# Performance work log

Hardware: AMD Instinct MI355X
Metric: run time of the kernel (lower is better)

The kernel has to match this reference:

```python
import jax, jax.numpy as jnp
import numpy as np

EMBED_DIM = 1024
NUM_HEADS = 16
HEAD_DIM = EMBED_DIM // NUM_HEADS
B, S = 2, 2048


def setup_inputs() -> dict:
    key = jax.random.key(0)
    k = jax.random.split(key, 8)
    scale = 1.0 / np.sqrt(EMBED_DIM)
    return {
        "x": jax.random.normal(k[0], (B, S, EMBED_DIM), dtype=jnp.float32),
        "x1": jax.random.normal(k[1], (B, S, EMBED_DIM), dtype=jnp.float32),
        "x2": jax.random.normal(k[2], (B, S, EMBED_DIM), dtype=jnp.float32),
        "qkv_w": jax.random.normal(k[3], (3 * EMBED_DIM, EMBED_DIM), dtype=jnp.float32) * scale,
        "qkv_b": jnp.zeros((3 * EMBED_DIM,), dtype=jnp.float32),
        "out_w": jax.random.normal(k[4], (EMBED_DIM, EMBED_DIM), dtype=jnp.float32) * scale,
        "out_b": jnp.zeros((EMBED_DIM,), dtype=jnp.float32),
    }


def reference(x, x1, x2, qkv_w, qkv_b, out_w, out_b):
    # x1, x2 are accepted but unused, matching the torch module.
    b, s, e = x.shape
    qkv = x @ qkv_w.T + qkv_b                      # [B,S,3E]
    qkv = qkv.reshape(b, s, 3, NUM_HEADS, HEAD_DIM)
    qkv = jnp.transpose(qkv, (2, 0, 3, 1, 4))      # [3,B,H,S,D]
    q, k, v = qkv[0], qkv[1], qkv[2]
    scores = jnp.einsum("bhqd,bhkd->bhqk", q, k) / np.sqrt(HEAD_DIM)
    probs = jax.nn.sigmoid(scores)                 # [B,H,S,S]
    sample = jax.random.bernoulli(jax.random.key(42), probs).astype(probs.dtype)
    # straight-through: forward uses sample, gradient flows as identity to probs
    attn = probs + jax.lax.stop_gradient(sample - probs)
    out = jnp.einsum("bhqk,bhkd->bhqd", attn, v)   # [B,H,S,D]
    out = jnp.transpose(out, (0, 2, 1, 3)).reshape(b, s, e)
    return out @ out_w.T + out_b
```

## Files before the change

kernel.cpp:

```cpp
#include <hip/hip_runtime.h>
#include <stdint.h>

#define NB 2
#define NS 2048
#define NE 1024
#define NH 16
#define ND 64

typedef __attribute__((ext_vector_type(8))) short short8;
typedef __attribute__((ext_vector_type(4))) float f4;
typedef __attribute__((ext_vector_type(4))) unsigned short us4;

static __device__ __forceinline__ unsigned short bf16_rne(float x) {
  uint32_t u = __builtin_bit_cast(uint32_t, x);
  u += 0x7fffu + ((u >> 16) & 1u);
  return (unsigned short)(u >> 16);
}
static __device__ __forceinline__ float bf16_f32(unsigned short h) {
  uint32_t u = ((uint32_t)h) << 16;
  return __builtin_bit_cast(float, u);
}

static __device__ __forceinline__ void threefry42(uint32_t x0, uint32_t x1,
                                                  uint32_t& o0, uint32_t& o1) {
  const uint32_t ks0 = 0u, ks1 = 42u;
  const uint32_t ks2 = 0u ^ 42u ^ 0x1BD11BDAu;
  x0 += ks0; x1 += ks1;
#define TF4(a,b,c,d) \
  x0 += x1; x1 = __builtin_rotateleft32(x1, a); x1 ^= x0; \
  x0 += x1; x1 = __builtin_rotateleft32(x1, b); x1 ^= x0; \
  x0 += x1; x1 = __builtin_rotateleft32(x1, c); x1 ^= x0; \
  x0 += x1; x1 = __builtin_rotateleft32(x1, d); x1 ^= x0;
  TF4(13,15,26,6)  x0 += ks1; x1 += ks2 + 1u;
  TF4(17,29,16,24) x0 += ks2; x1 += ks0 + 2u;
  TF4(13,15,26,6)  x0 += ks0; x1 += ks1 + 3u;
  TF4(17,29,16,24) x0 += ks1; x1 += ks2 + 4u;
  TF4(13,15,26,6)  x0 += ks2; x1 += ks0 + 5u;
#undef TF4
  o0 = x0; o1 = x1;
}

static __device__ __forceinline__ void gl2lds16(const void* g, void* l) {
  __builtin_amdgcn_global_load_lds(
      (const __attribute__((address_space(1))) uint32_t*)g,
      (__attribute__((address_space(3))) uint32_t*)l, 16, 0, 0);
}

__global__ void k_split(const float* __restrict__ x, const float* __restrict__ qw,
                        const float* __restrict__ ow,
                        unsigned short* __restrict__ xh, unsigned short* __restrict__ xl,
                        unsigned short* __restrict__ wh, unsigned short* __restrict__ wl,
                        unsigned short* __restrict__ woh) {
  for (uint32_t i = blockIdx.x * 256u + threadIdx.x; i < 8388608u; i += gridDim.x * 256u) {
    if (i < 4194304u) {
      float v = x[i];
      unsigned short hi = bf16_rne(v);
      xh[i] = hi;
      xl[i] = bf16_rne(v - bf16_f32(hi));
    } else if (i < 7340032u) {
      uint32_t j = i - 4194304u;
      float v = qw[j];
      unsigned short hi = bf16_rne(v);
      wh[j] = hi;
      wl[j] = bf16_rne(v - bf16_f32(hi));
    } else {
      uint32_t j = i - 7340032u;
      woh[j] = bf16_rne(ow[j]);
    }
  }
}

__global__ __launch_bounds__(256) void k_qkv(
    const unsigned short* __restrict__ xh, const unsigned short* __restrict__ xl,
    const unsigned short* __restrict__ wh, const unsigned short* __restrict__ wl,
    const float* __restrict__ qkv_b,
    unsigned short* __restrict__ Qh, unsigned short* __restrict__ Ql,
    unsigned short* __restrict__ Kh, unsigned short* __restrict__ Kl,
    unsigned short* __restrict__ Vt) {
  __shared__ unsigned short Ah[128 * 32], Al[128 * 32], Bh[128 * 32], Bl[128 * 32];
  const int tid = threadIdx.x;
  const int lane = tid & 63, wid = tid >> 6;
  const int wm = wid >> 1, wn = wid & 1;
  const int bn = blockIdx.x, bm = blockIdx.y;
  const int quad = lane >> 4, c16 = lane & 15;
  const int ldrow = lane >> 2;
  const int ldk = (lane & 3) * 8;

  f4 acc[4][4];
#pragma unroll
  for (int a = 0; a < 4; ++a)
#pragma unroll
    for (int b = 0; b < 4; ++b) { f4 z = {0.f, 0.f, 0.f, 0.f}; acc[a][b] = z; }

  for (int kt = 0; kt < 32; ++kt) {
    const int k0 = kt * 32;
    __syncthreads();
#pragma unroll
    for (int r = 0; r < 2; ++r) {
      const int c = wid + r * 4;
      const int grow = c * 16 + ldrow;
      const size_t ao = (size_t)(bm * 128 + grow) * 1024 + k0 + ldk;
      const size_t bo = (size_t)(bn * 128 + grow) * 1024 + k0 + ldk;
      const int lo = c * 512 + lane * 8;
      gl2lds16(xh + ao, &Ah[lo]);
      gl2lds16(xl + ao, &Al[lo]);
      gl2lds16(wh + bo, &Bh[lo]);
      gl2lds16(wl + bo, &Bl[lo]);
    }
    __syncthreads();

    short8 ah[4], al[4], bhf[4], blf[4];
#pragma unroll
    for (int t = 0; t < 4; ++t) {
      ah[t] = *(const short8*)&Ah[(wm * 64 + t * 16 + c16) * 32 + quad * 8];
      al[t] = *(const short8*)&Al[(wm * 64 + t * 16 + c16) * 32 + quad * 8];
      bhf[t] = *(const short8*)&Bh[(wn * 64 + t * 16 + c16) * 32 + quad * 8];
      blf[t] = *(const short8*)&Bl[(wn * 64 + t * 16 + c16) * 32 + quad * 8];
    }
#pragma unroll
    for (int tm = 0; tm < 4; ++tm)
#pragma unroll
      for (int tn = 0; tn < 4; ++tn) {
        acc[tm][tn] = __builtin_amdgcn_mfma_f32_16x16x32_bf16(ah[tm], bhf[tn], acc[tm][tn], 0, 0, 0);
        acc[tm][tn] = __builtin_amdgcn_mfma_f32_16x16x32_bf16(ah[tm], blf[tn], acc[tm][tn], 0, 0, 0);
        acc[tm][tn] = __builtin_amdgcn_mfma_f32_16x16x32_bf16(al[tm], bhf[tn], acc[tm][tn], 0, 0, 0);
      }
  }

#pragma unroll
  for (int tm = 0; tm < 4; ++tm) {
#pragma unroll
    for (int tn = 0; tn < 4; ++tn) {
      const int j = bn * 128 + wn * 64 + tn * 16 + c16;
      const float bias = qkv_b[j];
      const int which = j >> 10;
      const int rem = j & 1023;
      const int h = rem >> 6, d = rem & 63;
#pragma unroll
      for (int r = 0; r < 4; ++r) {
        const int i = bm * 128 + wm * 64 + tm * 16 + quad * 4 + r;
        const int b = i >> 11, s = i & 2047;
        const int bh = b * 16 + h;
        const float v = acc[tm][tn][r] + bias;
        if (which == 2) {
          Vt[((size_t)bh * 64 + d) * 2048 + s] = bf16_rne(v);
        } else {
          const size_t off = ((size_t)bh * 2048 + s) * 64 + d;
          const unsigned short hi = bf16_rne(v);
          const unsigned short lo = bf16_rne(v - bf16_f32(hi));
          if (which == 0) { Qh[off] = hi; Ql[off] = lo; }
          else            { Kh[off] = hi; Kl[off] = lo; }
        }
      }
    }
  }
}

__global__ __launch_bounds__(256) void k_attn(
    const unsigned short* __restrict__ Qh, const unsigned short* __restrict__ Ql,
    const unsigned short* __restrict__ Khg, const unsigned short* __restrict__ Klg,
    const unsigned short* __restrict__ Vtg, unsigned short* __restrict__ AO) {
  __shared__ unsigned short Ksh[4096], Ksl[4096], Vs[4096], Pm[4096];
  const int tid = threadIdx.x;
  const int lane = tid & 63, w = tid >> 6;
  const int quad = lane >> 4, c16 = lane & 15;
  const int q0 = blockIdx.x * 64;
  const int bh = blockIdx.y;
  const size_t base = (size_t)bh * (size_t)(2048 * 64);

  const size_t qoff = base + (size_t)(q0 + w * 16 + c16) * 64 + quad * 8;
  const short8 qh0 = *(const short8*)&Qh[qoff];
  const short8 qh1 = *(const short8*)&Qh[qoff + 32];
  const short8 ql0 = *(const short8*)&Ql[qoff];
  const short8 ql1 = *(const short8*)&Ql[qoff + 32];

  const uint32_t fb = (uint32_t)bh * 4194304u +
                      (uint32_t)(q0 + w * 16 + quad * 4) * 2048u + (uint32_t)c16;

  f4 oacc[4];
#pragma unroll
  for (int s = 0; s < 4; ++s) { f4 z = {0.f, 0.f, 0.f, 0.f}; oacc[s] = z; }

  for (int kt = 0; kt < 32; ++kt) {
    const int kb = kt * 64;
    const size_t koff = base + (size_t)kb * 64;
    __syncthreads();
#pragma unroll
    for (int rd = 0; rd < 2; ++rd) {
      const int lo = rd * 2048 + tid * 8;
      gl2lds16(Khg + koff + lo, &Ksh[lo]);
      gl2lds16(Klg + koff + lo, &Ksl[lo]);
      const int cid = rd * 256 + tid;
      const int vr = cid >> 3, vc = (cid & 7) * 8;
      gl2lds16(Vtg + base + (size_t)vr * 2048 + kb + vc, &Vs[cid * 8]);
    }
    __syncthreads();

    f4 sacc[4];
#pragma unroll
    for (int sub = 0; sub < 4; ++sub) {
      const int br = (sub * 16 + c16) * 64 + quad * 8;
      const short8 kh0 = *(const short8*)&Ksh[br];
      const short8 kh1 = *(const short8*)&Ksh[br + 32];
      const short8 kl0 = *(const short8*)&Ksl[br];
      const short8 kl1 = *(const short8*)&Ksl[br + 32];
      f4 s = {0.f, 0.f, 0.f, 0.f};
      s = __builtin_amdgcn_mfma_f32_16x16x32_bf16(qh0, kh0, s, 0, 0, 0);
      s = __builtin_amdgcn_mfma_f32_16x16x32_bf16(qh1, kh1, s, 0, 0, 0);
      s = __builtin_amdgcn_mfma_f32_16x16x32_bf16(qh0, kl0, s, 0, 0, 0);
      s = __builtin_amdgcn_mfma_f32_16x16x32_bf16(qh1, kl1, s, 0, 0, 0);
      s = __builtin_amdgcn_mfma_f32_16x16x32_bf16(ql0, kh0, s, 0, 0, 0);
      s = __builtin_amdgcn_mfma_f32_16x16x32_bf16(ql1, kh1, s, 0, 0, 0);
      sacc[sub] = s;
    }

#pragma unroll
    for (int sub = 0; sub < 4; ++sub) {
#pragma unroll
      for (int r = 0; r < 4; ++r) {
        const uint32_t f = fb + (uint32_t)(r * 2048) + (uint32_t)(kb + sub * 16);
        uint32_t o0, o1;
        threefry42(0u, f, o0, o1);
        const float m = (float)((o0 ^ o1) >> 9);
        const float e = __expf(sacc[sub][r] * -0.125f);
        const float p23 = 8388608.0f * __builtin_amdgcn_rcpf(1.0f + e);
        Pm[(w * 16 + quad * 4 + r) * 64 + sub * 16 + c16] = (m < p23) ? 0x3F80u : 0u;
      }
    }

    const int pr = (w * 16 + c16) * 64 + quad * 8;
    const short8 pa0 = *(const short8*)&Pm[pr];
    const short8 pa1 = *(const short8*)&Pm[pr + 32];
#pragma unroll
    for (int sub = 0; sub < 4; ++sub) {
      const int vr = (sub * 16 + c16) * 64 + quad * 8;
      const short8 vb0 = *(const short8*)&Vs[vr];
      const short8 vb1 = *(const short8*)&Vs[vr + 32];
      oacc[sub] = __builtin_amdgcn_mfma_f32_16x16x32_bf16(pa0, vb0, oacc[sub], 0, 0, 0);
      oacc[sub] = __builtin_amdgcn_mfma_f32_16x16x32_bf16(pa1, vb1, oacc[sub], 0, 0, 0);
    }
  }

  const int b = bh >> 4, hh = bh & 15;
#pragma unroll
  for (int sub = 0; sub < 4; ++sub)
#pragma unroll
    for (int r = 0; r < 4; ++r) {
      const int srow = b * 2048 + q0 + w * 16 + quad * 4 + r;
      AO[(size_t)srow * 1024 + hh * 64 + sub * 16 + c16] = bf16_rne(oacc[sub][r]);
    }
}

__global__ __launch_bounds__(256) void k_out(
    const unsigned short* __restrict__ A, const unsigned short* __restrict__ Bw,
    const float* __restrict__ out_b, float* __restrict__ out) {
  __shared__ unsigned short As[128 * 32], Bs[128 * 32];
  const int tid = threadIdx.x;
  const int lane = tid & 63, wid = tid >> 6;
  const int wm = wid >> 1, wn = wid & 1;
  const int bn = blockIdx.x, bm = blockIdx.y;
  const int quad = lane >> 4, c16 = lane & 15;
  const int ldrow = lane >> 2;
  const int ldk = (lane & 3) * 8;

  f4 acc[4][4];
#pragma unroll
  for (int a = 0; a < 4; ++a)
#pragma unroll
    for (int b = 0; b < 4; ++b) { f4 z = {0.f, 0.f, 0.f, 0.f}; acc[a][b] = z; }

  for (int kt = 0; kt < 32; ++kt) {
    const int k0 = kt * 32;
    __syncthreads();
#pragma unroll
    for (int r = 0; r < 2; ++r) {
      const int c = wid + r * 4;
      const int grow = c * 16 + ldrow;
      const size_t ao = (size_t)(bm * 128 + grow) * 1024 + k0 + ldk;
      const size_t bo = (size_t)(bn * 128 + grow) * 1024 + k0 + ldk;
      const int lo = c * 512 + lane * 8;
      gl2lds16(A + ao, &As[lo]);
      gl2lds16(Bw + bo, &Bs[lo]);
    }
    __syncthreads();

    short8 af[4], bf[4];
#pragma unroll
    for (int t = 0; t < 4; ++t) {
      af[t] = *(const short8*)&As[(wm * 64 + t * 16 + c16) * 32 + quad * 8];
      bf[t] = *(const short8*)&Bs[(wn * 64 + t * 16 + c16) * 32 + quad * 8];
    }
#pragma unroll
    for (int tm = 0; tm < 4; ++tm)
#pragma unroll
      for (int tn = 0; tn < 4; ++tn)
        acc[tm][tn] = __builtin_amdgcn_mfma_f32_16x16x32_bf16(af[tm], bf[tn], acc[tm][tn], 0, 0, 0);
  }

#pragma unroll
  for (int tm = 0; tm < 4; ++tm) {
#pragma unroll
    for (int tn = 0; tn < 4; ++tn) {
      const int j = bn * 128 + wn * 64 + tn * 16 + c16;
      const float bias = out_b[j];
#pragma unroll
      for (int r = 0; r < 4; ++r) {
        const int i = bm * 128 + wm * 64 + tm * 16 + quad * 4 + r;
        out[(size_t)i * 1024 + j] = acc[tm][tn][r] + bias;
      }
    }
  }
}

extern "C" void kernel_launch(void* const* d_in, const int* in_sizes, int n_in,
                              void* d_out, int out_size, void* d_ws, size_t ws_size,
                              hipStream_t stream) {
  const float* x     = (const float*)d_in[0];
  const float* qkv_w = (const float*)d_in[3];
  const float* qkv_b = (const float*)d_in[4];
  const float* out_w = (const float*)d_in[5];
  const float* out_b = (const float*)d_in[6];
  float* out = (float*)d_out;

  unsigned short* xh  = (unsigned short*)d_ws;
  unsigned short* xl  = xh + 4194304;
  unsigned short* wh  = xl + 4194304;
  unsigned short* wl  = wh + 3145728;
  unsigned short* woh = wl + 3145728;
  unsigned short* Vt  = woh + 1048576;
  unsigned short* Qh  = Vt + 4194304;
  unsigned short* Ql  = Qh + 4194304;
  unsigned short* Kh  = Ql + 4194304;
  unsigned short* Kl  = Kh + 4194304;
  unsigned short* AO  = xh;

  k_split<<<8192, 256, 0, stream>>>(x, qkv_w, out_w, xh, xl, wh, wl, woh);
  k_qkv<<<dim3(24, 32), 256, 0, stream>>>(xh, xl, wh, wl, qkv_b, Qh, Ql, Kh, Kl, Vt);
  k_attn<<<dim3(32, 32), 256, 0, stream>>>(Qh, Ql, Kh, Kl, Vt, AO);
  k_out<<<dim3(8, 32), 256, 0, stream>>>(AO, woh, out_b, out);
}
```

Measured before the change: 532.7 us.

## Prefetch K/V tiles during attention, swizzle LDS, skip split-bf16 for V projection

The attention kernel now copies each K/V tile from LDS into registers, then issues the global-to-LDS load for the next tile, so the copy overlaps with the QK MFMAs and the sigmoid/Bernoulli step. The K, V and P shared tiles use an XOR-style rotated layout to cut LDS bank conflicts. The sigmoid threshold test is rewritten to drop the reciprocal. In the QKV GEMM, V-column blocks skip the low-part bf16 loads and MFMAs, and V is transposed through LDS so Vt is written with coalesced 16-byte stores. The costs are higher register pressure from holding 24 short8 fragments, and V computed at lower precision. The rewritten comparison can also flip a sample at the boundary.

Result: faster. 520.2 us (-2.4%).

```diff
diff --git a/kernel.cpp b/kernel.cpp
--- a/kernel.cpp
+++ b/kernel.cpp
@@ -77,11 +77,16 @@
     unsigned short* __restrict__ Qh, unsigned short* __restrict__ Ql,
     unsigned short* __restrict__ Kh, unsigned short* __restrict__ Kl,
     unsigned short* __restrict__ Vt) {
-  __shared__ unsigned short Ah[128 * 32], Al[128 * 32], Bh[128 * 32], Bl[128 * 32];
+  __shared__ unsigned short SM[16384];
+  unsigned short* Ah = SM;
+  unsigned short* Al = SM + 4096;
+  unsigned short* Bh = SM + 8192;
+  unsigned short* Bl = SM + 12288;
   const int tid = threadIdx.x;
   const int lane = tid & 63, wid = tid >> 6;
   const int wm = wid >> 1, wn = wid & 1;
   const int bn = blockIdx.x, bm = blockIdx.y;
+  const bool isV = (bn >= 16);
   const int quad = lane >> 4, c16 = lane & 15;
   const int ldrow = lane >> 2;
   const int ldk = (lane & 3) * 8;
@@ -103,9 +108,11 @@
       const size_t bo = (size_t)(bn * 128 + grow) * 1024 + k0 + ldk;
       const int lo = c * 512 + lane * 8;
       gl2lds16(xh + ao, &Ah[lo]);
-      gl2lds16(xl + ao, &Al[lo]);
       gl2lds16(wh + bo, &Bh[lo]);
-      gl2lds16(wl + bo, &Bl[lo]);
+      if (!isV) {
+        gl2lds16(xl + ao, &Al[lo]);
+        gl2lds16(wl + bo, &Bl[lo]);
+      }
     }
     __syncthreads();
 
@@ -113,45 +120,82 @@
 #pragma unroll
     for (int t = 0; t < 4; ++t) {
       ah[t] = *(const short8*)&Ah[(wm * 64 + t * 16 + c16) * 32 + quad * 8];
-      al[t] = *(const short8*)&Al[(wm * 64 + t * 16 + c16) * 32 + quad * 8];
       bhf[t] = *(const short8*)&Bh[(wn * 64 + t * 16 + c16) * 32 + quad * 8];
-      blf[t] = *(const short8*)&Bl[(wn * 64 + t * 16 + c16) * 32 + quad * 8];
-    }
-#pragma unroll
-    for (int tm = 0; tm < 4; ++tm)
+      if (!isV) {
+        al[t] = *(const short8*)&Al[(wm * 64 + t * 16 + c16) * 32 + quad * 8];
+        blf[t] = *(const short8*)&Bl[(wn * 64 + t * 16 + c16) * 32 + quad * 8];
+      }
+    }
+    if (isV) {
+#pragma unroll
+      for (int tm = 0; tm < 4; ++tm)
+#pragma unroll
+        for (int tn = 0; tn < 4; ++tn)
+          acc[tm][tn] = __builtin_amdgcn_mfma_f32_16x16x32_bf16(ah[tm], bhf[tn], acc[tm][tn], 0, 0, 0);
+    } else {
+#pragma unroll
+      for (int tm = 0; tm < 4; ++tm)
+#pragma unroll
+        for (int tn = 0; tn < 4; ++tn) {
+          acc[tm][tn] = __builtin_amdgcn_mfma_f32_16x16x32_bf16(ah[tm], bhf[tn], acc[tm][tn], 0, 0, 0);
+          acc[tm][tn] = __builtin_amdgcn_mfma_f32_16x16x32_bf16(ah[tm], blf[tn], acc[tm][tn], 0, 0, 0);
+          acc[tm][tn] = __builtin_amdgcn_mfma_f32_16x16x32_bf16(al[tm], bhf[tn], acc[tm][tn], 0, 0, 0);
+        }
+    }
+  }
+
+  if (!isV) {
+#pragma unroll
+    for (int tm = 0; tm < 4; ++tm) {
 #pragma unroll
       for (int tn = 0; tn < 4; ++tn) {
-        acc[tm][tn] = __builtin_amdgcn_mfma_f32_16x16x32_bf16(ah[tm], bhf[tn], acc[tm][tn], 0, 0, 0);
-        acc[tm][tn] = __builtin_amdgcn_mfma_f32_16x16x32_bf16(ah[tm], blf[tn], acc[tm][tn], 0, 0, 0);
-        acc[tm][tn] = __builtin_amdgcn_mfma_f32_16x16x32_bf16(al[tm], bhf[tn], acc[tm][tn], 0, 0, 0);
-      }
-  }
-
-#pragma unroll
-  for (int tm = 0; tm < 4; ++tm) {
-#pragma unroll
-    for (int tn = 0; tn < 4; ++tn) {
-      const int j = bn * 128 + wn * 64 + tn * 16 + c16;
-      const float bias = qkv_b[j];
-      const int which = j >> 10;
-      const int rem = j & 1023;
-      const int h = rem >> 6, d = rem & 63;
-#pragma unroll
-      for (int r = 0; r < 4; ++r) {
-        const int i = bm * 128 + wm * 64 + tm * 16 + quad * 4 + r;
-        const int b = i >> 11, s = i & 2047;
-        const int bh = b * 16 + h;
-        const float v = acc[tm][tn][r] + bias;
-        if (which == 2) {
-          Vt[((size_t)bh * 64 + d) * 2048 + s] = bf16_rne(v);
-        } else {
-          const size_t off = ((size_t)bh * 2048 + s) * 64 + d;
+        const int j = bn * 128 + wn * 64 + tn * 16 + c16;
+        const float bias = qkv_b[j];
+        const int which = j >> 10;
+        const int rem = j & 1023;
+        const int h = rem >> 6, d = rem & 63;
+#pragma unroll
+        for (int r = 0; r < 4; ++r) {
+          const int i = bm * 128 + wm * 64 + tm * 16 + quad * 4 + r;
+          const int b = i >> 11, s = i & 2047;
+          const size_t off = (((size_t)(b * 16 + h)) * 2048 + (size_t)s) * 64 + d;
+          const float v = acc[tm][tn][r] + bias;
           const unsigned short hi = bf16_rne(v);
           const unsigned short lo = bf16_rne(v - bf16_f32(hi));
           if (which == 0) { Qh[off] = hi; Ql[off] = lo; }
           else            { Kh[off] = hi; Kl[off] = lo; }
         }
       }
+    }
+  } else {
+    __syncthreads();
+#pragma unroll
+    for (int tm = 0; tm < 4; ++tm) {
+#pragma unroll
+      for (int tn = 0; tn < 4; ++tn) {
+        const int j = bn * 128 + wn * 64 + tn * 16 + c16;
+        const float bias = qkv_b[j];
+        const int d_local = wn * 64 + tn * 16 + c16;
+#pragma unroll
+        for (int r = 0; r < 4; ++r) {
+          const int s_local = wm * 64 + tm * 16 + quad * 4 + r;
+          SM[d_local * 128 + s_local] = bf16_rne(acc[tm][tn][r] + bias);
+        }
+      }
+    }
+    __syncthreads();
+    const int b = (bm * 128) >> 11;
+    const int s0 = (bm * 128) & 2047;
+    const int h2 = (bn - 16) * 2;
+#pragma unroll
+    for (int it = 0; it < 8; ++it) {
+      const int chunk = it * 256 + tid;
+      const int dr = chunk >> 4;
+      const int sc = (chunk & 15) * 8;
+      const short8 v = *(const short8*)&SM[dr * 128 + sc];
+      const int bh = b * 16 + h2 + (dr >> 6);
+      const int d = dr & 63;
+      *(short8*)&Vt[((size_t)bh * 64 + d) * 2048 + s0 + sc] = v;
     }
   }
 }
@@ -177,67 +221,81 @@
   const uint32_t fb = (uint32_t)bh * 4194304u +
                       (uint32_t)(q0 + w * 16 + quad * 4) * 2048u + (uint32_t)c16;
 
+  const int c0 = tid, r0 = c0 >> 3, g0 = ((c0 & 7) - r0) & 7;
+  const int c1 = tid + 256, r1 = c1 >> 3, g1 = ((c1 & 7) - r1) & 7;
+
   f4 oacc[4];
 #pragma unroll
   for (int s = 0; s < 4; ++s) { f4 z = {0.f, 0.f, 0.f, 0.f}; oacc[s] = z; }
+
+  auto stage = [&](int kb) {
+    const size_t koff = base + (size_t)kb * 64;
+    gl2lds16(Khg + koff + r0 * 64 + g0 * 8, &Ksh[c0 * 8]);
+    gl2lds16(Klg + koff + r0 * 64 + g0 * 8, &Ksl[c0 * 8]);
+    gl2lds16(Vtg + base + (size_t)r0 * 2048 + kb + g0 * 8, &Vs[c0 * 8]);
+    gl2lds16(Khg + koff + r1 * 64 + g1 * 8, &Ksh[c1 * 8]);
+    gl2lds16(Klg + koff + r1 * 64 + g1 * 8, &Ksl[c1 * 8]);
+    gl2lds16(Vtg + base + (size_t)r1 * 2048 + kb + g1 * 8, &Vs[c1 * 8]);
+  };
+
+  stage(0);
 
   for (int kt = 0; kt < 32; ++kt) {
     const int kb = kt * 64;
-    const size_t koff = base + (size_t)kb * 64;
-    __syncthreads();
-#pragma unroll
-    for (int rd = 0; rd < 2; ++rd) {
-      const int lo = rd * 2048 + tid * 8;
-      gl2lds16(Khg + koff + lo, &Ksh[lo]);
-      gl2lds16(Klg + koff + lo, &Ksl[lo]);
-      const int cid = rd * 256 + tid;
-      const int vr = cid >> 3, vc = (cid & 7) * 8;
-      gl2lds16(Vtg + base + (size_t)vr * 2048 + kb + vc, &Vs[cid * 8]);
-    }
-    __syncthreads();
+    __syncthreads();
+
+    short8 kh[8], kl[8], vv[8];
+#pragma unroll
+    for (int sub = 0; sub < 4; ++sub) {
+      const int rK = sub * 16 + c16;
+      const int sA = ((quad + rK) & 7) * 8;
+      const int sB = ((quad + 4 + rK) & 7) * 8;
+      kh[2 * sub] = *(const short8*)&Ksh[rK * 64 + sA];
+      kh[2 * sub + 1] = *(const short8*)&Ksh[rK * 64 + sB];
+      kl[2 * sub] = *(const short8*)&Ksl[rK * 64 + sA];
+      kl[2 * sub + 1] = *(const short8*)&Ksl[rK * 64 + sB];
+      vv[2 * sub] = *(const short8*)&Vs[rK * 64 + sA];
+      vv[2 * sub + 1] = *(const short8*)&Vs[rK * 64 + sB];
+    }
+    __syncthreads();
+    if (kt < 31) stage(kb + 64);
 
     f4 sacc[4];
 #pragma unroll
     for (int sub = 0; sub < 4; ++sub) {
-      const int br = (sub * 16 + c16) * 64 + quad * 8;
-      const short8 kh0 = *(const short8*)&Ksh[br];
-      const short8 kh1 = *(const short8*)&Ksh[br + 32];
-      const short8 kl0 = *(const short8*)&Ksl[br];
-      const short8 kl1 = *(const short8*)&Ksl[br + 32];
       f4 s = {0.f, 0.f, 0.f, 0.f};
-      s = __builtin_amdgcn_mfma_f32_16x16x32_bf16(qh0, kh0, s, 0, 0, 0);
-      s = __builtin_amdgcn_mfma_f32_16x16x32_bf16(qh1, kh1, s, 0, 0, 0);
-      s = __builtin_amdgcn_mfma_f32_16x16x32_bf16(qh0, kl0, s, 0, 0, 0);
-      s = __builtin_amdgcn_mfma_f32_16x16x32_bf16(qh1, kl1, s, 0, 0, 0);
-      s = __builtin_amdgcn_mfma_f32_16x16x32_bf16(ql0, kh0, s, 0, 0, 0);
-      s = __builtin_amdgcn_mfma_f32_16x16x32_bf16(ql1, kh1, s, 0, 0, 0);
+      s = __builtin_amdgcn_mfma_f32_16x16x32_bf16(qh0, kh[2 * sub], s, 0, 0, 0);
+      s = __builtin_amdgcn_mfma_f32_16x16x32_bf16(qh1, kh[2 * sub + 1], s, 0, 0, 0);
+      s = __builtin_amdgcn_mfma_f32_16x16x32_bf16(qh0, kl[2 * sub], s, 0, 0, 0);
+      s = __builtin_amdgcn_mfma_f32_16x16x32_bf16(qh1, kl[2 * sub + 1], s, 0, 0, 0);
+      s = __builtin_amdgcn_mfma_f32_16x16x32_bf16(ql0, kh[2 * sub], s, 0, 0, 0);
+      s = __builtin_amdgcn_mfma_f32_16x16x32_bf16(ql1, kh[2 * sub + 1], s, 0, 0, 0);
       sacc[sub] = s;
     }
 
 #pragma unroll
     for (int sub = 0; sub < 4; ++sub) {
-#pragma unroll
-      for (int r = 0; r < 4; ++r) {
-        const uint32_t f = fb + (uint32_t)(r * 2048) + (uint32_t)(kb + sub * 16);
+      const int qP = sub * 2 + (c16 >> 3);
+#pragma unroll
+      for (int rr = 0; rr < 4; ++rr) {
+        const uint32_t f = fb + (uint32_t)(rr * 2048) + (uint32_t)(kb + sub * 16);
         uint32_t o0, o1;
         threefry42(0u, f, o0, o1);
         const float m = (float)((o0 ^ o1) >> 9);
-        const float e = __expf(sacc[sub][r] * -0.125f);
-        const float p23 = 8388608.0f * __builtin_amdgcn_rcpf(1.0f + e);
-        Pm[(w * 16 + quad * 4 + r) * 64 + sub * 16 + c16] = (m < p23) ? 0x3F80u : 0u;
-      }
-    }
-
-    const int pr = (w * 16 + c16) * 64 + quad * 8;
-    const short8 pa0 = *(const short8*)&Pm[pr];
-    const short8 pa1 = *(const short8*)&Pm[pr + 32];
+        const float e = __expf(sacc[sub][rr] * -0.125f);
+        const int rP = w * 16 + quad * 4 + rr;
+        const int addr = rP * 64 + (((qP + rP) & 7) * 8) + (c16 & 7);
+        Pm[addr] = (fmaf(m, e, m) < 8388608.0f) ? 0x3F80u : 0u;
+      }
+    }
+
+    const int rp = w * 16 + c16;
+    const short8 pa0 = *(const short8*)&Pm[rp * 64 + ((quad + rp) & 7) * 8];
+    const short8 pa1 = *(const short8*)&Pm[rp * 64 + ((quad + 4 + rp) & 7) * 8];
 #pragma unroll
     for (int sub = 0; sub < 4; ++sub) {
-      const int vr = (sub * 16 + c16) * 64 + quad * 8;
-      const short8 vb0 = *(const short8*)&Vs[vr];
-      const short8 vb1 = *(const short8*)&Vs[vr + 32];
-      oacc[sub] = __builtin_amdgcn_mfma_f32_16x16x32_bf16(pa0, vb0, oacc[sub], 0, 0, 0);
-      oacc[sub] = __builtin_amdgcn_mfma_f32_16x16x32_bf16(pa1, vb1, oacc[sub], 0, 0, 0);
+      oacc[sub] = __builtin_amdgcn_mfma_f32_16x16x32_bf16(pa0, vv[2 * sub], oacc[sub], 0, 0, 0);
+      oacc[sub] = __builtin_amdgcn_mfma_f32_16x16x32_bf16(pa1, vv[2 * sub + 1], oacc[sub], 0, 0, 0);
     }
   }
 
```
